# Optimization experiments

Hardware: AMD Instinct MI355X
Metric: run time of the kernel (lower is better)

Reference implementation:

```python
import jax, jax.numpy as jnp
import numpy as np

EMB = 2048
H = 16        # num query heads
G = 4         # num kv groups (kv heads)
GS = H // G   # group size = 4
HD = EMB // H # head dim = 128
B, T = 2, 2048


def setup_inputs() -> dict:
    key = jax.random.key(0)
    ks = jax.random.split(key, 6)
    s = 1.0 / np.sqrt(EMB)
    return {
        "x": jax.random.normal(ks[0], (B, T, EMB), dtype=jnp.float32),
        "Wq": jax.random.normal(ks[1], (EMB, EMB), dtype=jnp.float32) * s,
        "Wk": jax.random.normal(ks[2], (EMB, EMB), dtype=jnp.float32) * s,
        "Wv": jax.random.normal(ks[3], (EMB, EMB), dtype=jnp.float32) * s,
        "Wp": jax.random.normal(ks[4], (EMB, EMB), dtype=jnp.float32) * s,
        "bp": jnp.zeros((EMB,), dtype=jnp.float32),
    }


def reference(x, Wq, Wk, Wv, Wp, bp):
    # Dropout layers (p=0.5) treated as identity (eval mode) for a deterministic baseline.
    b, t, c = x.shape
    # torch nn.Linear: y = x @ W.T
    q = (x @ Wq.T).reshape(b, t, G, GS, HD)          # head h = g*GS + s
    q = q.transpose(0, 2, 3, 1, 4)                   # (B, G, GS, T, HD)
    # GQA: keys/values use only the first head of each group, then broadcast
    # over the GS query heads of that group (equivalent to repeat_interleave).
    k = (x @ Wk.T).reshape(b, t, G, GS, HD)[:, :, :, 0, :].transpose(0, 2, 1, 3)  # (B, G, T, HD)
    v = (x @ Wv.T).reshape(b, t, G, GS, HD)[:, :, :, 0, :].transpose(0, 2, 1, 3)  # (B, G, T, HD)

    scale = HD ** (-0.5)
    scores = jnp.einsum('bgsqd,bgkd->bgsqk', q, k) * scale  # (B,G,GS,T,T)
    causal = jnp.tril(jnp.ones((t, t), dtype=bool))
    scores = jnp.where(causal, scores, -jnp.inf)
    attn = jax.nn.softmax(scores, axis=-1)
    out = jnp.einsum('bgsqk,bgkd->bgsqd', attn, v)           # (B,G,GS,T,HD)
    out = out.transpose(0, 3, 1, 2, 4).reshape(b, t, c)       # heads back in h=g*GS+s order
    return out @ Wp.T + bp
```

## Files before the change

### kernel.cpp

```cpp
#include <hip/hip_runtime.h>
#include <hip/hip_bf16.h>


typedef unsigned short ushort_t;
typedef __bf16 bf16x8 __attribute__((ext_vector_type(8)));
typedef float f32x4 __attribute__((ext_vector_type(4)));

__device__ __forceinline__ ushort_t f2bf(float f) {
  union { float f; unsigned u; } x; x.f = f;
  unsigned r = x.u + 0x7fffu + ((x.u >> 16) & 1u);
  return (ushort_t)(r >> 16);
}

__device__ __forceinline__ void cast_plain(const float* __restrict__ in,
                                           ushort_t* __restrict__ out, int i) {
  float4 v = reinterpret_cast<const float4*>(in)[i];
  ushort4 o;
  o.x = f2bf(v.x); o.y = f2bf(v.y); o.z = f2bf(v.z); o.w = f2bf(v.w);
  reinterpret_cast<ushort4*>(out)[i] = o;
}
__device__ __forceinline__ void cast_cmp(const float* __restrict__ in,
                                         ushort_t* __restrict__ out, int i) {
  int row = i >> 9, c = i & 511;
  int srow = ((row >> 7) << 9) | (row & 127);
  float4 v = reinterpret_cast<const float4*>(in + (size_t)srow * 2048)[c];
  ushort4 o;
  o.x = f2bf(v.x); o.y = f2bf(v.y); o.z = f2bf(v.z); o.w = f2bf(v.w);
  reinterpret_cast<ushort4*>(out + (size_t)row * 2048)[c] = o;
}
__global__ __launch_bounds__(256) void cast_all(const float* __restrict__ x,
                                                const float* __restrict__ Wq,
                                                const float* __restrict__ Wk,
                                                const float* __restrict__ Wv,
                                                const float* __restrict__ Wp,
                                                ushort_t* __restrict__ xb,
                                                ushort_t* __restrict__ wqkb,
                                                ushort_t* __restrict__ wvb,
                                                ushort_t* __restrict__ wpb) {
  int bid = blockIdx.x, tid = threadIdx.x;
  if (bid < 8192)       cast_plain(x,  xb,  bid * 256 + tid);
  else if (bid < 12288) cast_plain(Wq, wqkb, (bid - 8192) * 256 + tid);
  else if (bid < 16384) cast_plain(Wp, wpb, (bid - 12288) * 256 + tid);
  else if (bid < 17408) cast_cmp(Wk, wqkb + (size_t)2048 * 2048, (bid - 16384) * 256 + tid);
  else                  cast_cmp(Wv, wvb, (bid - 17408) * 256 + tid);
}

template<bool FINAL>
__device__ __forceinline__ void gemm_tile(ushort_t* __restrict__ lA,
                                          ushort_t* __restrict__ lB,
                                          const ushort_t* __restrict__ A,
                                          const ushort_t* __restrict__ B,
                                          ushort_t* __restrict__ Cb,
                                          float* __restrict__ Cf,
                                          const float* __restrict__ bias,
                                          int m0, int n0, int N, int K) {
  const int lane = threadIdx.x & 63;
  const int w = threadIdx.x >> 6;
  const int wm = (w >> 1) * 64, wn = (w & 1) * 64;
  const int l4 = lane >> 4, l15 = lane & 15;

  const f32x4 zero = {0.f, 0.f, 0.f, 0.f};
  f32x4 acc[4][4];
#pragma unroll
  for (int i = 0; i < 4; ++i)
#pragma unroll
    for (int j = 0; j < 4; ++j) acc[i][j] = zero;

  const int srow = w * 8 + (lane >> 3);
  const int scol = ((lane & 7) ^ (lane >> 3)) * 8;
  const ushort_t* ga = A + (size_t)(m0 + srow) * K + scol;
  const ushort_t* gb = B + (size_t)(n0 + srow) * K + scol;

  for (int kt = 0; kt < K; kt += 64) {
#pragma unroll
    for (int i = 0; i < 4; ++i) {
      __builtin_amdgcn_global_load_lds(
          (const __attribute__((address_space(1))) void*)(ga + (size_t)i * 32 * K + kt),
          (__attribute__((address_space(3))) void*)(&lA[i * 2048 + w * 512]), 16, 0, 0);
      __builtin_amdgcn_global_load_lds(
          (const __attribute__((address_space(1))) void*)(gb + (size_t)i * 32 * K + kt),
          (__attribute__((address_space(3))) void*)(&lB[i * 2048 + w * 512]), 16, 0, 0);
    }
    __syncthreads();
#pragma unroll
    for (int kk = 0; kk < 2; ++kk) {
      bf16x8 af[4], bfr[4];
#pragma unroll
      for (int t = 0; t < 4; ++t) {
        const int Ra = wm + t * 16 + l15;
        const int Rb = wn + t * 16 + l15;
        af[t]  = *reinterpret_cast<const bf16x8*>(&lA[Ra * 64 + ((kk * 4 + l4) ^ (Ra & 7)) * 8]);
        bfr[t] = *reinterpret_cast<const bf16x8*>(&lB[Rb * 64 + ((kk * 4 + l4) ^ (Rb & 7)) * 8]);
      }
#pragma unroll
      for (int mi = 0; mi < 4; ++mi)
#pragma unroll
        for (int ni = 0; ni < 4; ++ni)
          acc[mi][ni] = __builtin_amdgcn_mfma_f32_16x16x32_bf16(af[mi], bfr[ni],
                                                                acc[mi][ni], 0, 0, 0);
    }
    __syncthreads();
  }

#pragma unroll
  for (int mi = 0; mi < 4; ++mi)
#pragma unroll
    for (int ni = 0; ni < 4; ++ni) {
      int row = m0 + wm + mi * 16 + l4 * 4;
      int col = n0 + wn + ni * 16 + l15;
#pragma unroll
      for (int r = 0; r < 4; ++r) {
        float v = acc[mi][ni][r];
        if (FINAL) Cf[(size_t)(row + r) * N + col] = v + bias[col];
        else       Cb[(size_t)(row + r) * N + col] = f2bf(v);
      }
    }
}

__global__ __launch_bounds__(256) void proj_fused(const ushort_t* __restrict__ xb,
                                                  const ushort_t* __restrict__ wqkb,
                                                  const ushort_t* __restrict__ wvb,
                                                  ushort_t* __restrict__ qkbuf,
                                                  ushort_t* __restrict__ vtb) {
  __shared__ ushort_t lA[128 * 64];
  __shared__ ushort_t lB[128 * 64];
  int bid = blockIdx.x;
  if (bid < 640) {
    gemm_tile<false>(lA, lB, xb, wqkb, qkbuf, nullptr, nullptr,
                     (bid / 20) * 128, (bid % 20) * 128, 2560, 2048);
  } else {
    int t = bid - 640;
    gemm_tile<false>(lA, lB, wvb, xb, vtb, nullptr, nullptr,
                     (t / 32) * 128, (t % 32) * 128, 4096, 2048);
  }
}

__global__ __launch_bounds__(256) void gemm_final(const ushort_t* __restrict__ A,
                                                  const ushort_t* __restrict__ B,
                                                  float* __restrict__ Cf,
                                                  const float* __restrict__ bias) {
  __shared__ ushort_t lA[128 * 64];
  __shared__ ushort_t lB[128 * 64];
  gemm_tile<true>(lA, lB, A, B, nullptr, Cf, bias,
                  (int)blockIdx.y * 128, (int)blockIdx.x * 128, 2048, 2048);
}

__global__ __launch_bounds__(256, 2) void attn_kernel(const ushort_t* __restrict__ Qb, int ldQ,
                                                      const ushort_t* __restrict__ Kb, int ldK,
                                                      const ushort_t* __restrict__ Vt,
                                                      ushort_t* __restrict__ Ob) {
  __shared__ ushort_t ldsK[2][64 * 128];
  __shared__ ushort_t ldsV[2][128 * 64];
  __shared__ ushort_t pbuf[4][16 * 72];

  const int lane = threadIdx.x & 63;
  const int w = threadIdx.x >> 6;
  const int swz = ((blockIdx.x & 7) << 6) | (blockIdx.x >> 3);
  const int b = swz >> 8, hq = (swz >> 4) & 15, pair = swz & 15;
  const int g = hq >> 2;
  const int l4 = lane >> 4, l15 = lane & 15;
  const int tau_hi = 31 - pair, tau_lo = pair;
  const int hi_iters = tau_hi + 1;
  const int total_iters = hi_iters + tau_lo + 1;
  const float C = 0.12751744f;

  const int krow = w * 4 + (lane >> 4);
  const ushort_t* kBase = Kb + (size_t)(b * 2048 + krow) * ldK + g * 128 + ((lane & 15) ^ (krow & 7)) * 8;
  const int vrow = w * 8 + (lane >> 3);
  const ushort_t* vBase = Vt + (size_t)(g * 128 + vrow) * 4096 + b * 2048 + ((lane & 7) ^ (vrow & 7)) * 8;

  const f32x4 zero = {0.f, 0.f, 0.f, 0.f};
  f32x4 o[8];
  float mr[4], lr[4];
  bf16x8 qf[4];

  auto LOADQ = [&](int tau) {
    const ushort_t* qp = Qb + (size_t)(b * 2048 + tau * 64 + w * 16 + l15) * ldQ + hq * 128 + l4 * 8;
#pragma unroll
    for (int kk = 0; kk < 4; ++kk) {
      bf16x8 q = *reinterpret_cast<const bf16x8*>(qp + kk * 32);
#pragma unroll
      for (int j = 0; j < 8; ++j) q[j] = (__bf16)((float)q[j] * C);
      qf[kk] = q;
    }
  };
  auto RESET = [&]() {
#pragma unroll
    for (int i = 0; i < 8; ++i) o[i] = zero;
#pragma unroll
    for (int r = 0; r < 4; ++r) { mr[r] = -3.0e38f; lr[r] = 0.f; }
  };
  auto STAGE = [&](int tt, int bc) {
    const int js = (tt < hi_iters) ? tt * 64 : (tt - hi_iters) * 64;
    const ushort_t* ks = kBase + (size_t)js * ldK;
    const ushort_t* vs = vBase + js;
#pragma unroll
    for (int i = 0; i < 4; ++i) {
      __builtin_amdgcn_global_load_lds(
          (const __attribute__((address_space(1))) void*)(ks + (size_t)i * 16 * ldK),
          (__attribute__((address_space(3))) void*)(&ldsK[bc][i * 2048 + w * 512]), 16, 0, 0);
      __builtin_amdgcn_global_load_lds(
          (const __attribute__((address_space(1))) void*)(vs + (size_t)i * 32 * 4096),
          (__attribute__((address_space(3))) void*)(&ldsV[bc][i * 2048 + w * 512]), 16, 0, 0);
    }
  };
  auto FINALIZE = [&](int tau) {
#pragma unroll
    for (int r = 0; r < 4; ++r) {
#pragma unroll
      for (int d = 1; d < 16; d <<= 1) lr[r] += __shfl_xor(lr[r], d, 16);
      lr[r] = 1.0f / lr[r];
    }
    ushort_t* op = Ob + (size_t)(b * 2048 + tau * 64 + w * 16) * 2048 + hq * 128;
#pragma unroll
    for (int ni = 0; ni < 8; ++ni)
#pragma unroll
      for (int r = 0; r < 4; ++r)
        op[(size_t)(l4 * 4 + r) * 2048 + ni * 16 + l15] = f2bf(o[ni][r] * lr[r]);
  };

  RESET();
  LOADQ(tau_hi);
  STAGE(0, 0);

  for (int t = 0; t < total_iters; ++t) {
    if (t == hi_iters) {
      FINALIZE(tau_hi);
      RESET();
      LOADQ(tau_lo);
    }
    __syncthreads();
    if (t + 1 < total_iters) STAGE(t + 1, (t + 1) & 1);
    const int bc = t & 1;

    const int tau = (t < hi_iters) ? tau_hi : tau_lo;
    const int tloc = (t < hi_iters) ? t : (t - hi_iters);
    const int j0 = tloc * 64;
    const int q0 = tau * 64 + w * 16;
    const bool diag = (tloc == tau);

    f32x4 s[4];
#pragma unroll
    for (int i = 0; i < 4; ++i) s[i] = zero;
#pragma unroll
    for (int ni = 0; ni < 4; ++ni) {
      const int R = ni * 16 + l15;
#pragma unroll
      for (int kk = 0; kk < 4; ++kk) {
        bf16x8 kf = *reinterpret_cast<const bf16x8*>(
            &ldsK[bc][R * 128 + ((kk * 4 + l4) ^ (R & 7)) * 8]);
        s[ni] = __builtin_amdgcn_mfma_f32_16x16x32_bf16(qf[kk], kf, s[ni], 0, 0, 0);
      }
    }
    float pmax[4] = {-3.0e38f, -3.0e38f, -3.0e38f, -3.0e38f};
    if (diag) {
#pragma unroll
      for (int ni = 0; ni < 4; ++ni) {
        int col = j0 + ni * 16 + l15;
#pragma unroll
        for (int r = 0; r < 4; ++r) {
          int qq = q0 + l4 * 4 + r;
          float v = (col <= qq) ? s[ni][r] : -3.0e38f;
          s[ni][r] = v;
          pmax[r] = fmaxf(pmax[r], v);
        }
      }
    } else {
#pragma unroll
      for (int ni = 0; ni < 4; ++ni)
#pragma unroll
        for (int r = 0; r < 4; ++r) pmax[r] = fmaxf(pmax[r], s[ni][r]);
    }
    bool small = (pmax[0] <= mr[0] + 8.f) & (pmax[1] <= mr[1] + 8.f) &
                 (pmax[2] <= mr[2] + 8.f) & (pmax[3] <= mr[3] + 8.f);
    if (!__all(small)) {
#pragma unroll
      for (int r = 0; r < 4; ++r) {
#pragma unroll
        for (int d = 1; d < 16; d <<= 1) pmax[r] = fmaxf(pmax[r], __shfl_xor(pmax[r], d, 16));
        float mn = fmaxf(mr[r], pmax[r]);
        float corr = exp2f(mr[r] - mn);
        mr[r] = mn;
        lr[r] *= corr;
#pragma unroll
        for (int i = 0; i < 8; ++i) o[i][r] *= corr;
      }
    }
#pragma unroll
    for (int ni = 0; ni < 4; ++ni)
#pragma unroll
      for (int r = 0; r < 4; ++r) {
        float p = exp2f(s[ni][r] - mr[r]);
        lr[r] += p;
        pbuf[w][(l4 * 4 + r) * 72 + ni * 16 + l15] = f2bf(p);
      }
    bf16x8 pa[2];
#pragma unroll
    for (int kk2 = 0; kk2 < 2; ++kk2)
      pa[kk2] = *reinterpret_cast<const bf16x8*>(&pbuf[w][l15 * 72 + kk2 * 32 + l4 * 8]);
#pragma unroll
    for (int ni = 0; ni < 8; ++ni) {
      const int R = ni * 16 + l15;
#pragma unroll
      for (int kk2 = 0; kk2 < 2; ++kk2) {
        bf16x8 vf = *reinterpret_cast<const bf16x8*>(
            &ldsV[bc][R * 64 + ((kk2 * 4 + l4) ^ (R & 7)) * 8]);
        o[ni] = __builtin_amdgcn_mfma_f32_16x16x32_bf16(pa[kk2], vf, o[ni], 0, 0, 0);
      }
    }
  }
  FINALIZE(tau_lo);
}

extern "C" void kernel_launch(void* const* d_in, const int* in_sizes, int n_in,
                              void* d_out, int out_size, void* d_ws, size_t ws_size,
                              hipStream_t stream) {
  const float* x  = (const float*)d_in[0];
  const float* Wq = (const float*)d_in[1];
  const float* Wk = (const float*)d_in[2];
  const float* Wv = (const float*)d_in[3];
  const float* Wp = (const float*)d_in[4];
  const float* bp = (const float*)d_in[5];
  float* out = (float*)d_out;

  char* ws = (char*)d_ws;
  size_t off = 0;
  ushort_t* xb    = (ushort_t*)(ws + off); off += (size_t)4096 * 2048 * 2;
  ushort_t* wqkb  = (ushort_t*)(ws + off); off += (size_t)2560 * 2048 * 2;
  ushort_t* wvb   = (ushort_t*)(ws + off); off += (size_t)512 * 2048 * 2;
  ushort_t* wpb   = (ushort_t*)(ws + off); off += (size_t)2048 * 2048 * 2;
  ushort_t* qkbuf = (ushort_t*)(ws + off); off += (size_t)4096 * 2560 * 2;
  ushort_t* vtb   = (ushort_t*)(ws + off); off += (size_t)512 * 4096 * 2;
  ushort_t* obuf  = (ushort_t*)(ws + off); off += (size_t)4096 * 2048 * 2;

  cast_all<<<18432, 256, 0, stream>>>(x, Wq, Wk, Wv, Wp, xb, wqkb, wvb, wpb);

  proj_fused<<<768, 256, 0, stream>>>(xb, wqkb, wvb, qkbuf, vtb);

  attn_kernel<<<512, 256, 0, stream>>>(qkbuf, 2560, qkbuf + 2048, 2560, vtb, obuf);

  gemm_final<<<dim3(16, 32), 256, 0, stream>>>(obuf, wpb, out, bp);
}
```

Before: 307.3 us.

## Fuse four stages into a persistent cooperative mega-kernel with grid syncs

Replaces the four separate launches (cast, QKV projection, attention, output projection) with one cooperative kernel of 512 persistent blocks that loop over each stage's work units and separate the stages with grid-wide barriers. The aim is to remove launch gaps and tail effects between kernels. In exchange, the cast and projection stages run with fewer resident blocks, and every block carries the largest LDS footprint and register budget of any stage. An occupancy check falls back to the old multi-launch path if two blocks per CU cannot be resident.

Result: no change. 312.6 us (+1.7%).

```diff
diff --git a/kernel.cpp b/kernel.cpp
--- a/kernel.cpp
+++ b/kernel.cpp
@@ -1,5 +1,8 @@
 #include <hip/hip_runtime.h>
 #include <hip/hip_bf16.h>
+#include <hip/hip_cooperative_groups.h>
+
+namespace cg = cooperative_groups;
 
 
 typedef unsigned short ushort_t;
@@ -28,21 +31,16 @@
   o.x = f2bf(v.x); o.y = f2bf(v.y); o.z = f2bf(v.z); o.w = f2bf(v.w);
   reinterpret_cast<ushort4*>(out + (size_t)row * 2048)[c] = o;
 }
-__global__ __launch_bounds__(256) void cast_all(const float* __restrict__ x,
-                                                const float* __restrict__ Wq,
-                                                const float* __restrict__ Wk,
-                                                const float* __restrict__ Wv,
-                                                const float* __restrict__ Wp,
-                                                ushort_t* __restrict__ xb,
-                                                ushort_t* __restrict__ wqkb,
-                                                ushort_t* __restrict__ wvb,
-                                                ushort_t* __restrict__ wpb) {
-  int bid = blockIdx.x, tid = threadIdx.x;
-  if (bid < 8192)       cast_plain(x,  xb,  bid * 256 + tid);
-  else if (bid < 12288) cast_plain(Wq, wqkb, (bid - 8192) * 256 + tid);
-  else if (bid < 16384) cast_plain(Wp, wpb, (bid - 12288) * 256 + tid);
-  else if (bid < 17408) cast_cmp(Wk, wqkb + (size_t)2048 * 2048, (bid - 16384) * 256 + tid);
-  else                  cast_cmp(Wv, wvb, (bid - 17408) * 256 + tid);
+__device__ __forceinline__ void cast_unit(int u, int tid,
+                                          const float* x, const float* Wq, const float* Wk,
+                                          const float* Wv, const float* Wp,
+                                          ushort_t* xb, ushort_t* wqkb,
+                                          ushort_t* wvb, ushort_t* wpb) {
+  if (u < 8192)       cast_plain(x,  xb,  u * 256 + tid);
+  else if (u < 12288) cast_plain(Wq, wqkb, (u - 8192) * 256 + tid);
+  else if (u < 16384) cast_plain(Wp, wpb, (u - 12288) * 256 + tid);
+  else if (u < 17408) cast_cmp(Wk, wqkb + (size_t)2048 * 2048, (u - 16384) * 256 + tid);
+  else                cast_cmp(Wv, wvb, (u - 17408) * 256 + tid);
 }
 
 template<bool FINAL>
@@ -117,44 +115,30 @@
     }
 }
 
-__global__ __launch_bounds__(256) void proj_fused(const ushort_t* __restrict__ xb,
-                                                  const ushort_t* __restrict__ wqkb,
-                                                  const ushort_t* __restrict__ wvb,
-                                                  ushort_t* __restrict__ qkbuf,
-                                                  ushort_t* __restrict__ vtb) {
-  __shared__ ushort_t lA[128 * 64];
-  __shared__ ushort_t lB[128 * 64];
-  int bid = blockIdx.x;
-  if (bid < 640) {
+__device__ __forceinline__ void proj_unit(int t, ushort_t* lA, ushort_t* lB,
+                                          const ushort_t* xb, const ushort_t* wqkb,
+                                          const ushort_t* wvb, ushort_t* qkbuf,
+                                          ushort_t* vtb) {
+  if (t < 640) {
     gemm_tile<false>(lA, lB, xb, wqkb, qkbuf, nullptr, nullptr,
-                     (bid / 20) * 128, (bid % 20) * 128, 2560, 2048);
+                     (t / 20) * 128, (t % 20) * 128, 2560, 2048);
   } else {
-    int t = bid - 640;
+    int u = t - 640;
     gemm_tile<false>(lA, lB, wvb, xb, vtb, nullptr, nullptr,
-                     (t / 32) * 128, (t % 32) * 128, 4096, 2048);
+                     (u / 32) * 128, (u % 32) * 128, 4096, 2048);
   }
 }
 
-__global__ __launch_bounds__(256) void gemm_final(const ushort_t* __restrict__ A,
-                                                  const ushort_t* __restrict__ B,
-                                                  float* __restrict__ Cf,
-                                                  const float* __restrict__ bias) {
-  __shared__ ushort_t lA[128 * 64];
-  __shared__ ushort_t lB[128 * 64];
-  gemm_tile<true>(lA, lB, A, B, nullptr, Cf, bias,
-                  (int)blockIdx.y * 128, (int)blockIdx.x * 128, 2048, 2048);
-}
-
-__global__ __launch_bounds__(256, 2) void attn_kernel(const ushort_t* __restrict__ Qb, int ldQ,
-                                                      const ushort_t* __restrict__ Kb, int ldK,
-                                                      const ushort_t* __restrict__ Vt,
-                                                      ushort_t* __restrict__ Ob) {
-  __shared__ ushort_t ldsK[2][64 * 128];
-  __shared__ ushort_t ldsV[2][128 * 64];
-  __shared__ ushort_t pbuf[4][16 * 72];
-
+__device__ __forceinline__ void attn_body(ushort_t* __restrict__ ldsK,
+                                          ushort_t* __restrict__ ldsV,
+                                          ushort_t* __restrict__ pbufA,
+                                          const ushort_t* __restrict__ Qb, int ldQ,
+                                          const ushort_t* __restrict__ Kb, int ldK,
+                                          const ushort_t* __restrict__ Vt,
+                                          ushort_t* __restrict__ Ob) {
   const int lane = threadIdx.x & 63;
   const int w = threadIdx.x >> 6;
+  ushort_t* pbuf = pbufA + w * 1152;
   const int swz = ((blockIdx.x & 7) << 6) | (blockIdx.x >> 3);
   const int b = swz >> 8, hq = (swz >> 4) & 15, pair = swz & 15;
   const int g = hq >> 2;
@@ -198,10 +182,10 @@
     for (int i = 0; i < 4; ++i) {
       __builtin_amdgcn_global_load_lds(
           (const __attribute__((address_space(1))) void*)(ks + (size_t)i * 16 * ldK),
-          (__attribute__((address_space(3))) void*)(&ldsK[bc][i * 2048 + w * 512]), 16, 0, 0);
+          (__attribute__((address_space(3))) void*)(&ldsK[bc * 8192 + i * 2048 + w * 512]), 16, 0, 0);
       __builtin_amdgcn_global_load_lds(
           (const __attribute__((address_space(1))) void*)(vs + (size_t)i * 32 * 4096),
-          (__attribute__((address_space(3))) void*)(&ldsV[bc][i * 2048 + w * 512]), 16, 0, 0);
+          (__attribute__((address_space(3))) void*)(&ldsV[bc * 8192 + i * 2048 + w * 512]), 16, 0, 0);
     }
   };
   auto FINALIZE = [&](int tau) {
@@ -248,7 +232,7 @@
 #pragma unroll
       for (int kk = 0; kk < 4; ++kk) {
         bf16x8 kf = *reinterpret_cast<const bf16x8*>(
-            &ldsK[bc][R * 128 + ((kk * 4 + l4) ^ (R & 7)) * 8]);
+            &ldsK[bc * 8192 + R * 128 + ((kk * 4 + l4) ^ (R & 7)) * 8]);
         s[ni] = __builtin_amdgcn_mfma_f32_16x16x32_bf16(qf[kk], kf, s[ni], 0, 0, 0);
       }
     }
@@ -292,24 +276,90 @@
       for (int r = 0; r < 4; ++r) {
         float p = exp2f(s[ni][r] - mr[r]);
         lr[r] += p;
-        pbuf[w][(l4 * 4 + r) * 72 + ni * 16 + l15] = f2bf(p);
+        pbuf[(l4 * 4 + r) * 72 + ni * 16 + l15] = f2bf(p);
       }
     bf16x8 pa[2];
 #pragma unroll
     for (int kk2 = 0; kk2 < 2; ++kk2)
-      pa[kk2] = *reinterpret_cast<const bf16x8*>(&pbuf[w][l15 * 72 + kk2 * 32 + l4 * 8]);
+      pa[kk2] = *reinterpret_cast<const bf16x8*>(&pbuf[l15 * 72 + kk2 * 32 + l4 * 8]);
 #pragma unroll
     for (int ni = 0; ni < 8; ++ni) {
       const int R = ni * 16 + l15;
 #pragma unroll
       for (int kk2 = 0; kk2 < 2; ++kk2) {
         bf16x8 vf = *reinterpret_cast<const bf16x8*>(
-            &ldsV[bc][R * 64 + ((kk2 * 4 + l4) ^ (R & 7)) * 8]);
+            &ldsV[bc * 8192 + R * 64 + ((kk2 * 4 + l4) ^ (R & 7)) * 8]);
         o[ni] = __builtin_amdgcn_mfma_f32_16x16x32_bf16(pa[kk2], vf, o[ni], 0, 0, 0);
       }
     }
   }
   FINALIZE(tau_lo);
+}
+
+__global__ __launch_bounds__(256, 2) void mega_kernel(
+    const float* __restrict__ x, const float* __restrict__ Wq,
+    const float* __restrict__ Wk, const float* __restrict__ Wv,
+    const float* __restrict__ Wp, const float* __restrict__ bp,
+    float* __restrict__ out,
+    ushort_t* xb, ushort_t* wqkb, ushort_t* wvb, ushort_t* wpb,
+    ushort_t* qkbuf, ushort_t* vtb, ushort_t* obuf) {
+  extern __shared__ ushort_t smem[];
+  cg::grid_group gg = cg::this_grid();
+  const int tid = threadIdx.x;
+
+  for (int u = blockIdx.x; u < 18432; u += 512)
+    cast_unit(u, tid, x, Wq, Wk, Wv, Wp, xb, wqkb, wvb, wpb);
+  gg.sync();
+
+  for (int t = blockIdx.x; t < 768; t += 512)
+    proj_unit(t, smem, smem + 8192, xb, wqkb, wvb, qkbuf, vtb);
+  gg.sync();
+
+  attn_body(smem, smem + 16384, smem + 32768,
+            qkbuf, 2560, qkbuf + 2048, 2560, vtb, obuf);
+  gg.sync();
+
+  gemm_tile<true>(smem, smem + 8192, obuf, wpb, nullptr, out, bp,
+                  ((int)blockIdx.x >> 4) * 128, ((int)blockIdx.x & 15) * 128,
+                  2048, 2048);
+}
+
+__global__ __launch_bounds__(256) void cast_all(const float* __restrict__ x,
+                                                const float* __restrict__ Wq,
+                                                const float* __restrict__ Wk,
+                                                const float* __restrict__ Wv,
+                                                const float* __restrict__ Wp,
+                                                ushort_t* __restrict__ xb,
+                                                ushort_t* __restrict__ wqkb,
+                                                ushort_t* __restrict__ wvb,
+                                                ushort_t* __restrict__ wpb) {
+  cast_unit(blockIdx.x, threadIdx.x, x, Wq, Wk, Wv, Wp, xb, wqkb, wvb, wpb);
+}
+
+__global__ __launch_bounds__(256) void proj_fused(const ushort_t* __restrict__ xb,
+                                                  const ushort_t* __restrict__ wqkb,
+                                                  const ushort_t* __restrict__ wvb,
+                                                  ushort_t* __restrict__ qkbuf,
+                                                  ushort_t* __restrict__ vtb) {
+  __shared__ ushort_t lds[2 * 128 * 64];
+  proj_unit(blockIdx.x, lds, lds + 8192, xb, wqkb, wvb, qkbuf, vtb);
+}
+
+__global__ __launch_bounds__(256, 2) void attn_kernel(const ushort_t* __restrict__ Qb, int ldQ,
+                                                      const ushort_t* __restrict__ Kb, int ldK,
+                                                      const ushort_t* __restrict__ Vt,
+                                                      ushort_t* __restrict__ Ob) {
+  __shared__ ushort_t s[37376];
+  attn_body(s, s + 16384, s + 32768, Qb, ldQ, Kb, ldK, Vt, Ob);
+}
+
+__global__ __launch_bounds__(256) void gemm_final(const ushort_t* __restrict__ A,
+                                                  const ushort_t* __restrict__ B,
+                                                  float* __restrict__ Cf,
+                                                  const float* __restrict__ bias) {
+  __shared__ ushort_t lds[2 * 128 * 64];
+  gemm_tile<true>(lds, lds + 8192, A, B, nullptr, Cf, bias,
+                  (int)blockIdx.y * 128, (int)blockIdx.x * 128, 2048, 2048);
 }
 
 extern "C" void kernel_launch(void* const* d_in, const int* in_sizes, int n_in,
@@ -333,11 +383,18 @@
   ushort_t* vtb   = (ushort_t*)(ws + off); off += (size_t)512 * 4096 * 2;
   ushort_t* obuf  = (ushort_t*)(ws + off); off += (size_t)4096 * 2048 * 2;
 
-  cast_all<<<18432, 256, 0, stream>>>(x, Wq, Wk, Wv, Wp, xb, wqkb, wvb, wpb);
-
-  proj_fused<<<768, 256, 0, stream>>>(xb, wqkb, wvb, qkbuf, vtb);
-
-  attn_kernel<<<512, 256, 0, stream>>>(qkbuf, 2560, qkbuf + 2048, 2560, vtb, obuf);
-
-  gemm_final<<<dim3(16, 32), 256, 0, stream>>>(obuf, wpb, out, bp);
-}
+  int nb = 0;
+  hipOccupancyMaxActiveBlocksPerMultiprocessor(&nb, mega_kernel, 256, (size_t)74752);
+  if (nb >= 2) {
+    void* args[] = {(void*)&x, (void*)&Wq, (void*)&Wk, (void*)&Wv, (void*)&Wp,
+                    (void*)&bp, (void*)&out, (void*)&xb, (void*)&wqkb, (void*)&wvb,
+                    (void*)&wpb, (void*)&qkbuf, (void*)&vtb, (void*)&obuf};
+    hipLaunchCooperativeKernel(mega_kernel, dim3(512), dim3(256), args,
+                               (unsigned)74752, stream);
+  } else {
+    cast_all<<<18432, 256, 0, stream>>>(x, Wq, Wk, Wv, Wp, xb, wqkb, wvb, wpb);
+    proj_fused<<<768, 256, 0, stream>>>(xb, wqkb, wvb, qkbuf, vtb);
+    attn_kernel<<<512, 256, 0, stream>>>(qkbuf, 2560, qkbuf + 2048, 2560, vtb, obuf);
+    gemm_final<<<dim3(16, 32), 256, 0, stream>>>(obuf, wpb, out, bp);
+  }
+}
```
